# Kernel tuning notes

Hardware: AMD Instinct MI355X
Metric: run time of the kernel (lower is better)

## Reference

```python
import jax, jax.numpy as jnp
import numpy as np

N_NODES = 50000
N_EDGES = 800000
D = 128          # input_dim == output_dim
H = 2 * D        # hidden size = 2*output_dim
EPS = 1e-5       # BatchNorm1d eps


def _mlp(x, W1, b1, g1, beta1, W2, b2):
    # Linear -> BatchNorm1d (training-mode batch stats) -> ReLU -> Linear
    y = x @ W1 + b1
    mu = jnp.mean(y, axis=0)
    var = jnp.mean(jnp.square(y - mu), axis=0)  # biased var, as used for normalization
    y = (y - mu) * jax.lax.rsqrt(var + EPS) * g1 + beta1
    y = jax.nn.relu(y)
    return y @ W2 + b2


def setup_inputs() -> dict:
    key = jax.random.key(0)
    ks = jax.random.split(key, 16)
    h = jax.random.normal(ks[0], (N_NODES, D), dtype=jnp.float32)
    e = jax.random.normal(ks[1], (N_EDGES, D), dtype=jnp.float32)
    src = jax.random.randint(ks[2], (N_EDGES,), 0, N_NODES, dtype=jnp.int32)
    dst = jax.random.randint(ks[3], (N_EDGES,), 0, N_NODES, dtype=jnp.int32)

    def lin(k, fan_in, fan_out):
        return jax.random.normal(k, (fan_in, fan_out), dtype=jnp.float32) * (1.0 / np.sqrt(fan_in))

    params = {
        # mlp_bond: in 2D -> H -> D
        'W1b': lin(ks[4], 2 * D, H), 'b1b': jnp.zeros((H,), jnp.float32),
        'g1b': jnp.ones((H,), jnp.float32), 'beta1b': jnp.zeros((H,), jnp.float32),
        'W2b': lin(ks[5], H, D), 'b2b': jnp.zeros((D,), jnp.float32),
        # mlp_atom: in 2D -> H -> D
        'W1a': lin(ks[6], 2 * D, H), 'b1a': jnp.zeros((H,), jnp.float32),
        'g1a': jnp.ones((H,), jnp.float32), 'beta1a': jnp.zeros((H,), jnp.float32),
        'W2a': lin(ks[7], H, D), 'b2a': jnp.zeros((D,), jnp.float32),
    }
    return {'h': h, 'e': e, 'src': src, 'dst': dst, **params}


def reference(h, e, src, dst,
              W1b, b1b, g1b, beta1b, W2b, b2b,
              W1a, b1a, g1a, beta1a, W2a, b2a):
    # --- bond update: gather u_add_v, concat with e, MLP ---
    sum_h_edge = h[src] + h[dst]                              # [E, D]
    e_new = _mlp(jnp.concatenate([sum_h_edge, e], axis=-1),
                 W1b, b1b, g1b, beta1b, W2b, b2b)             # [E, D]

    # --- atom update: scatter-sum of src node feats and NEW edge feats to dst ---
    sum_h = jax.ops.segment_sum(h[src], dst, num_segments=N_NODES)   # copy_u + sum
    sum_e = jax.ops.segment_sum(e_new, dst, num_segments=N_NODES)   # copy_e + sum
    h_new = _mlp(jnp.concatenate([sum_h, sum_e], axis=-1),
                 W1a, b1a, g1a, beta1a, W2a, b2a)             # [N, D]

    # out_batch_norm=False, out_activation=None, residual=False, dropout=None
    return h_new, e_new
```

## Files before the change

kernel.cpp:

```cpp
#include <hip/hip_runtime.h>
#include <stdint.h>

#define DD 128
#define HH 256
#define EPSBN 1e-5f

typedef __attribute__((ext_vector_type(4))) float f32x4;
typedef __attribute__((ext_vector_type(8))) short s16x8;
typedef __attribute__((ext_vector_type(4))) short s16x4;

__device__ __forceinline__ unsigned short f2bf(float f){
  union{float f; unsigned u;} v; v.f=f;
  unsigned u = v.u + 0x7fffu + ((v.u>>16)&1u);
  return (unsigned short)(u>>16);
}
__device__ __forceinline__ float bf2f(unsigned short s){
  union{unsigned u; float f;} v; v.u=((unsigned)s)<<16; return v.f;
}
__device__ __forceinline__ int swz(int row, int kb){ return row*512 + (kb ^ ((row&7)<<4)); }

__global__ void wt_kernel(const float* __restrict__ W1b, const float* __restrict__ W2b,
                          const float* __restrict__ W1a, const float* __restrict__ W2a,
                          unsigned short* __restrict__ WT1b, unsigned short* __restrict__ WT2b,
                          unsigned short* __restrict__ WT1a, unsigned short* __restrict__ WT2a){
  int idx = blockIdx.x*256 + threadIdx.x;
  if (idx < 65536){ int n=idx>>8, k=idx&255; WT1b[n*256+k]=f2bf(W1b[k*256+n]); }
  else if (idx < 98304){ int t=idx-65536; int n=t>>8, k=t&255; WT2b[n*256+k]=f2bf(W2b[k*128+n]); }
  else if (idx < 163840){ int t=idx-98304; int n=t>>8, k=t&255; WT1a[n*256+k]=f2bf(W1a[k*256+n]); }
  else if (idx < 196608){ int t=idx-163840; int n=t>>8, k=t&255; WT2a[n*256+k]=f2bf(W2a[k*128+n]); }
}

__global__ void h2bf_kernel(const float* __restrict__ h, unsigned short* __restrict__ hb, int n8){
  int i = blockIdx.x*256 + threadIdx.x;
  if (i < n8){
    f32x4 a = *(const f32x4*)(h + (size_t)i*8);
    f32x4 b = *(const f32x4*)(h + (size_t)i*8 + 4);
    s16x8 p;
    #pragma unroll
    for (int q=0;q<4;q++){ p[q]=(short)f2bf(a[q]); p[4+q]=(short)f2bf(b[q]); }
    *(s16x8*)(hb + (size_t)i*8) = p;
  }
}

__global__ void hist_kernel(const int* __restrict__ dst, int* __restrict__ counts, int E){
  int i = blockIdx.x*256 + threadIdx.x;
  if (i < E) atomicAdd(&counts[dst[i]], 1);
}

__global__ void scan_kernel(const int* __restrict__ counts, int* __restrict__ offsets,
                            int* __restrict__ cursor, int n){
  __shared__ int wsum[16];
  int tid = threadIdx.x, lane = tid&63, wid = tid>>6;
  int carry = 0;
  int nch = (n + 1023)/1024;
  for (int ch=0; ch<nch; ch++){
    int i = ch*1024 + tid;
    int v = (i<n)? counts[i] : 0;
    int s = v;
    #pragma unroll
    for (int off=1; off<64; off<<=1){ int t = __shfl_up(s, off); if (lane>=off) s += t; }
    if (lane==63) wsum[wid] = s;
    __syncthreads();
    int woff = 0, tot = 0;
    #pragma unroll
    for (int w=0; w<16; w++){ int t = wsum[w]; if (w<wid) woff += t; tot += t; }
    if (i<n){ int excl = carry + woff + s - v; offsets[i]=excl; cursor[i]=excl; }
    carry += tot;
    __syncthreads();
  }
  if (tid==0) offsets[n] = carry;
}

__global__ void fill_kernel(const int* __restrict__ dst, int* __restrict__ cursor,
                            int* __restrict__ eids, int E){
  int i = blockIdx.x*256 + threadIdx.x;
  if (i < E){ int slot = atomicAdd(&cursor[dst[i]], 1); eids[slot] = i; }
}

__device__ __forceinline__ void gemm1_core(char* xt, const s16x8 (&Bf)[8][2],
                                           float bias0, float bias1,
                                           unsigned short* __restrict__ yout,
                                           float* __restrict__ stats,
                                           int base, int nrows)
{
  const int tid = threadIdx.x;
  const int l = tid&63, w = tid>>6, lr = l&15, lg = l>>4;
  const int nb = w*32;
  f32x4 acc[4][2];
  #pragma unroll
  for (int mt=0;mt<4;mt++)
    #pragma unroll
    for (int nt=0;nt<2;nt++) acc[mt][nt] = (f32x4){0.f,0.f,0.f,0.f};
  #pragma unroll
  for (int kc=0;kc<8;kc++){
    s16x8 af[4];
    #pragma unroll
    for (int mt=0;mt<4;mt++)
      af[mt] = *(const s16x8*)(xt + swz(mt*16 + lr, kc*64 + lg*16));
    #pragma unroll
    for (int nt=0;nt<2;nt++)
      #pragma unroll
      for (int mt=0;mt<4;mt++)
        acc[mt][nt] = __builtin_amdgcn_mfma_f32_16x16x32_bf16(af[mt], Bf[kc][nt], acc[mt][nt], 0,0,0);
  }
  float st1a=0.f, st1b=0.f, st2a=0.f, st2b=0.f;
  #pragma unroll
  for (int mt=0;mt<4;mt++)
    #pragma unroll
    for (int q=0;q<4;q++){
      float m = (base + mt*16 + lg*4 + q < nrows) ? 1.0f : 0.0f;
      float v0 = (acc[mt][0][q] + bias0)*m;
      float v1 = (acc[mt][1][q] + bias1)*m;
      st1a += v0; st2a += v0*v0;
      st1b += v1; st2b += v1*v1;
    }
  __syncthreads();
  #pragma unroll
  for (int mt=0;mt<4;mt++)
    #pragma unroll
    for (int q=0;q<4;q++){
      *(unsigned short*)(xt + (mt*16 + lg*4 + q)*512 + (nb + lr)*2)      = f2bf(acc[mt][0][q] + bias0);
      *(unsigned short*)(xt + (mt*16 + lg*4 + q)*512 + (nb + 16 + lr)*2) = f2bf(acc[mt][1][q] + bias1);
    }
  __syncthreads();
  #pragma unroll
  for (int it=0;it<4;it++){
    int off = it*8192 + tid*16;
    int row = off >> 9;
    if (base + row < nrows)
      *(s16x8*)((char*)yout + (size_t)base*512 + off) = *(const s16x8*)(xt + off);
  }
  {
    int rep = blockIdx.x & 63;
    float s;
    s = st1a; s += __shfl_xor(s,16); s += __shfl_xor(s,32);
    if (l < 16) atomicAdd(&stats[rep*512 + nb + lr], s);
    s = st2a; s += __shfl_xor(s,16); s += __shfl_xor(s,32);
    if (l < 16) atomicAdd(&stats[rep*512 + 256 + nb + lr], s);
    s = st1b; s += __shfl_xor(s,16); s += __shfl_xor(s,32);
    if (l < 16) atomicAdd(&stats[rep*512 + nb + 16 + lr], s);
    s = st2b; s += __shfl_xor(s,16); s += __shfl_xor(s,32);
    if (l < 16) atomicAdd(&stats[rep*512 + 256 + nb + 16 + lr], s);
  }
}

__global__ __launch_bounds__(512, 4) void edge_mlp1(
    const unsigned short* __restrict__ hb, const float* __restrict__ e,
    const int* __restrict__ src, const int* __restrict__ dstv,
    const unsigned short* __restrict__ WT1, const float* __restrict__ b1,
    unsigned short* __restrict__ yout, float* __restrict__ stats, int E)
{
  __shared__ alignas(16) char xt[32768];
  const int tid = threadIdx.x;
  const int l = tid&63, w = tid>>6, lr = l&15, lg = l>>4;
  const int nb = w*32;
  const int base = blockIdx.x*64;

  {
    const int cb = tid&31, r0 = tid>>5;
    #pragma unroll
    for (int k=0;k<4;k++){
      int r = r0 + k*16;
      f32x4 v = *(const f32x4*)(e + (size_t)(base+r)*DD + cb*4);
      s16x4 p;
      #pragma unroll
      for (int q=0;q<4;q++) p[q] = (short)f2bf(v[q]);
      *(s16x4*)(xt + swz(r, 256 + cb*8)) = p;
    }
  }
  {
    const int r = tid>>3, jj = tid&7;
    const int ei = base + r;
    int s_ = src[ei], d_ = dstv[ei];
    const s16x8* hs = (const s16x8*)(hb + (size_t)s_*DD) + jj*2;
    const s16x8* hd = (const s16x8*)(hb + (size_t)d_*DD) + jj*2;
    s16x8 a0=hs[0], a1=hs[1], c0=hd[0], c1=hd[1];
    s16x8 o0, o1;
    #pragma unroll
    for (int q=0;q<8;q++){
      o0[q] = (short)f2bf(bf2f((unsigned short)a0[q]) + bf2f((unsigned short)c0[q]));
      o1[q] = (short)f2bf(bf2f((unsigned short)a1[q]) + bf2f((unsigned short)c1[q]));
    }
    *(s16x8*)(xt + swz(r, jj*32))      = o0;
    *(s16x8*)(xt + swz(r, jj*32 + 16)) = o1;
  }
  s16x8 Bf[8][2];
  #pragma unroll
  for (int kc=0;kc<8;kc++)
    #pragma unroll
    for (int nt=0;nt<2;nt++)
      Bf[kc][nt] = *(const s16x8*)(WT1 + (size_t)(nb + nt*16 + lr)*256 + kc*32 + lg*8);
  float bias0 = b1[nb+lr], bias1 = b1[nb+16+lr];
  __syncthreads();
  gemm1_core(xt, Bf, bias0, bias1, yout, stats, base, E);
}

__global__ __launch_bounds__(512, 2) void node_mlp1(
    const unsigned short* __restrict__ hb, const float* __restrict__ enew,
    const int* __restrict__ src, const int* __restrict__ offsets, const int* __restrict__ eids,
    const unsigned short* __restrict__ WT1, const float* __restrict__ b1,
    unsigned short* __restrict__ yout, float* __restrict__ stats, int NN)
{
  __shared__ alignas(16) char xt[32768];
  const int tid = threadIdx.x;
  const int l = tid&63, w = tid>>6, lr = l&15, lg = l>>4;
  const int nb = w*32;
  const int base = blockIdx.x*64;
  const int r = tid>>3, jj = tid&7;
  const int node = base + r;

  float ah[16], ae[16];
  #pragma unroll
  for (int q=0;q<16;q++){ ah[q]=0.f; ae[q]=0.f; }
  if (node < NN){
    int beg = offsets[node], end = offsets[node+1];
    for (int p=beg;p<end;p++){
      int eid = eids[p];
      int s_ = src[eid];
      const s16x8* hs = (const s16x8*)(hb + (size_t)s_*DD + jj*16);
      const f32x4* ep = (const f32x4*)(enew + (size_t)eid*DD + jj*16);
      s16x8 a0 = hs[0], a1 = hs[1];
      f32x4 e0 = ep[0], e1 = ep[1], e2 = ep[2], e3 = ep[3];
      #pragma unroll
      for (int q=0;q<8;q++){ ah[q] += bf2f((unsigned short)a0[q]); ah[8+q] += bf2f((unsigned short)a1[q]); }
      #pragma unroll
      for (int q=0;q<4;q++){ ae[q] += e0[q]; ae[4+q] += e1[q]; ae[8+q] += e2[q]; ae[12+q] += e3[q]; }
    }
  }
  {
    s16x8 o0, o1;
    #pragma unroll
    for (int q=0;q<8;q++){ o0[q] = (short)f2bf(ah[q]); o1[q] = (short)f2bf(ah[8+q]); }
    *(s16x8*)(xt + swz(r, jj*32))      = o0;
    *(s16x8*)(xt + swz(r, jj*32 + 16)) = o1;
    #pragma unroll
    for (int q=0;q<8;q++){ o0[q] = (short)f2bf(ae[q]); o1[q] = (short)f2bf(ae[8+q]); }
    *(s16x8*)(xt + swz(r, 256 + jj*32))      = o0;
    *(s16x8*)(xt + swz(r, 256 + jj*32 + 16)) = o1;
  }
  s16x8 Bf[8][2];
  #pragma unroll
  for (int kc=0;kc<8;kc++)
    #pragma unroll
    for (int nt=0;nt<2;nt++)
      Bf[kc][nt] = *(const s16x8*)(WT1 + (size_t)(nb + nt*16 + lr)*256 + kc*32 + lg*8);
  float bias0 = b1[nb+lr], bias1 = b1[nb+16+lr];
  __syncthreads();
  gemm1_core(xt, Bf, bias0, bias1, yout, stats, base, NN);
}

__global__ void finalize_kernel(const float* __restrict__ stats, const float* __restrict__ g,
                                const float* __restrict__ beta, float* __restrict__ scale, float invcnt){
  __shared__ float red[512];
  int tid = threadIdx.x;
  float s = 0.f;
  for (int rep=0; rep<64; rep++) s += stats[rep*512 + tid];
  red[tid] = s;
  __syncthreads();
  if (tid < 256){
    float mu  = red[tid]*invcnt;
    float var = red[256+tid]*invcnt - mu*mu;
    float a = g[tid] * rsqrtf(var + EPSBN);
    float c = beta[tid] - mu*a;
    scale[2*tid] = a; scale[2*tid+1] = c;
  }
}

__global__ __launch_bounds__(512, 4) void mlp2_kernel(const unsigned short* y,
    const unsigned short* __restrict__ WT2, const float* __restrict__ b2,
    const float* __restrict__ scale, float* outp, int nrows)
{
  __shared__ alignas(16) char xt[32768];
  const int tid = threadIdx.x;
  const int l = tid&63, w = tid>>6, lr = l&15, lg = l>>4;
  const int nb = w*16;
  const int base = blockIdx.x*64;

  const int cb = tid&31, r0 = tid>>5;
  float sa[8], sc[8];
  #pragma unroll
  for (int q=0;q<8;q++){ sa[q]=scale[2*(cb*8+q)]; sc[q]=scale[2*(cb*8+q)+1]; }
  #pragma unroll
  for (int k=0;k<4;k++){
    int r = r0 + k*16;
    s16x8 raw = {0,0,0,0,0,0,0,0};
    if (base + r < nrows) raw = *(const s16x8*)(y + (size_t)(base+r)*HH + cb*8);
    s16x8 o;
    #pragma unroll
    for (int q=0;q<8;q++){
      float f = fmaxf(bf2f((unsigned short)raw[q])*sa[q] + sc[q], 0.0f);
      o[q] = (short)f2bf(f);
    }
    *(s16x8*)(xt + swz(r, cb*16)) = o;
  }
  s16x8 Bf[8];
  #pragma unroll
  for (int kc=0;kc<8;kc++)
    Bf[kc] = *(const s16x8*)(WT2 + (size_t)(nb + lr)*HH + kc*32 + lg*8);
  float bias = b2[nb+lr];
  __syncthreads();

  f32x4 acc[4];
  #pragma unroll
  for (int mt=0;mt<4;mt++) acc[mt] = (f32x4){0.f,0.f,0.f,0.f};
  #pragma unroll
  for (int kc=0;kc<8;kc++){
    s16x8 af[4];
    #pragma unroll
    for (int mt=0;mt<4;mt++)
      af[mt] = *(const s16x8*)(xt + swz(mt*16 + lr, kc*64 + lg*16));
    #pragma unroll
    for (int mt=0;mt<4;mt++)
      acc[mt] = __builtin_amdgcn_mfma_f32_16x16x32_bf16(af[mt], Bf[kc], acc[mt], 0,0,0);
  }
  __syncthreads();
  #pragma unroll
  for (int mt=0;mt<4;mt++)
    #pragma unroll
    for (int q=0;q<4;q++)
      *(float*)(xt + (mt*16 + lg*4 + q)*512 + (nb + lr)*4) = acc[mt][q] + bias;
  __syncthreads();
  #pragma unroll
  for (int it=0;it<4;it++){
    int off = it*8192 + tid*16;
    int row = off >> 9;
    if (base + row < nrows)
      *(f32x4*)(outp + (size_t)(base+row)*DD + ((off&511)>>2)) = *(const f32x4*)(xt + off);
  }
}

extern "C" void kernel_launch(void* const* d_in, const int* in_sizes, int n_in,
                              void* d_out, int out_size, void* d_ws, size_t ws_size,
                              hipStream_t stream) {
  const float* h    = (const float*)d_in[0];
  const float* e    = (const float*)d_in[1];
  const int*   src  = (const int*)d_in[2];
  const int*   dst  = (const int*)d_in[3];
  const float* W1b  = (const float*)d_in[4];
  const float* b1b  = (const float*)d_in[5];
  const float* g1b  = (const float*)d_in[6];
  const float* beta1b=(const float*)d_in[7];
  const float* W2b  = (const float*)d_in[8];
  const float* b2b  = (const float*)d_in[9];
  const float* W1a  = (const float*)d_in[10];
  const float* b1a  = (const float*)d_in[11];
  const float* g1a  = (const float*)d_in[12];
  const float* beta1a=(const float*)d_in[13];
  const float* W2a  = (const float*)d_in[14];
  const float* b2a  = (const float*)d_in[15];

  const int E  = in_sizes[2];
  const int NN = in_sizes[0] / DD;

  char* ws = (char*)d_ws;
  unsigned short* WT1b = (unsigned short*)(ws + 0);
  unsigned short* WT2b = (unsigned short*)(ws + 131072);
  unsigned short* WT1a = (unsigned short*)(ws + 196608);
  unsigned short* WT2a = (unsigned short*)(ws + 327680);
  float* scaleE = (float*)(ws + 393216);
  float* scaleN = (float*)(ws + 395264);
  float* statsE = (float*)(ws + 397312);
  float* statsN = (float*)(ws + 528384);
  int* counts  = (int*)(ws + 659456);
  int* offsets = (int*)(ws + 860160);
  int* cursor  = (int*)(ws + 1060864);
  int* eids    = (int*)(ws + 1261568);
  unsigned short* ya = (unsigned short*)(ws + 4461568);
  unsigned short* hb = (unsigned short*)(ws + 30086144);

  float* outH = (float*)d_out;
  float* outE = outH + (size_t)NN * DD;
  unsigned short* yE = (unsigned short*)outE;

  hipMemsetAsync(ws + 397312, 0, 131072 + 131072 + 200704, stream);

  wt_kernel<<<768, 256, 0, stream>>>(W1b, W2b, W1a, W2a, WT1b, WT2b, WT1a, WT2a);
  h2bf_kernel<<<(NN*DD/8 + 255)/256, 256, 0, stream>>>(h, hb, NN*DD/8);
  hist_kernel<<<(E+255)/256, 256, 0, stream>>>(dst, counts, E);
  scan_kernel<<<1, 1024, 0, stream>>>(counts, offsets, cursor, NN);
  fill_kernel<<<(E+255)/256, 256, 0, stream>>>(dst, cursor, eids, E);

  const int tE = E/64;
  const int tN = (NN + 63)/64;

  edge_mlp1<<<tE, 512, 0, stream>>>(hb, e, src, dst, WT1b, b1b, yE, statsE, E);
  finalize_kernel<<<1, 512, 0, stream>>>(statsE, g1b, beta1b, scaleE, 1.0f/(float)E);
  mlp2_kernel<<<tE, 512, 0, stream>>>(yE, WT2b, b2b, scaleE, outE, E);
  node_mlp1<<<tN, 512, 0, stream>>>(hb, outE, src, offsets, eids, WT1a, b1a, ya, statsN, NN);
  finalize_kernel<<<1, 512, 0, stream>>>(statsN, g1a, beta1a, scaleN, 1.0f/(float)NN);
  mlp2_kernel<<<tN, 512, 0, stream>>>(ya, WT2a, b2a, scaleN, outH, NN);
}
```

Baseline: 800.5 us.

## Recompute edge GEMM1 instead of storing hidden; fuse MLP2 with atomic scatter-sum

The edge MLP now runs in two passes. The first pass computes only the BatchNorm statistics of the first linear layer. The second pass recomputes the gather and GEMM1, then applies BN, ReLU and GEMM2 in one fused kernel. It writes e_new and atomically scatter-adds it into a per-node sum buffer, so the node kernel no longer gathers e_new per edge. This drops the bf16 hidden-activation round trip and the CSR gather of edge features, at the cost of a duplicated gather plus GEMM1 and 800k×128 float atomics. It also swaps the manual bf16 rounding for the library conversion.

```diff
diff --git a/kernel.cpp b/kernel.cpp
--- a/kernel.cpp
+++ b/kernel.cpp
@@ -1,4 +1,5 @@
 #include <hip/hip_runtime.h>
+#include <hip/hip_bf16.h>
 #include <stdint.h>
 
 #define DD 128
@@ -10,9 +11,9 @@
 typedef __attribute__((ext_vector_type(4))) short s16x4;
 
 __device__ __forceinline__ unsigned short f2bf(float f){
-  union{float f; unsigned u;} v; v.f=f;
-  unsigned u = v.u + 0x7fffu + ((v.u>>16)&1u);
-  return (unsigned short)(u>>16);
+  union { __hip_bfloat16 h; unsigned short u; } v;
+  v.h = __float2bfloat16(f);
+  return v.u;
 }
 __device__ __forceinline__ float bf2f(unsigned short s){
   union{unsigned u; float f;} v; v.u=((unsigned)s)<<16; return v.f;
@@ -75,6 +76,199 @@
                             int* __restrict__ eids, int E){
   int i = blockIdx.x*256 + threadIdx.x;
   if (i < E){ int slot = atomicAdd(&cursor[dst[i]], 1); eids[slot] = i; }
+}
+
+__device__ __forceinline__ void stage_edge_tile(char* xt,
+    const unsigned short* __restrict__ hb, const float* __restrict__ e,
+    const int* __restrict__ src, const int* __restrict__ dstv, int base)
+{
+  const int tid = threadIdx.x;
+  {
+    const int cb = tid&31, r0 = tid>>5;
+    #pragma unroll
+    for (int k=0;k<4;k++){
+      int r = r0 + k*16;
+      f32x4 v = *(const f32x4*)(e + (size_t)(base+r)*DD + cb*4);
+      s16x4 p;
+      #pragma unroll
+      for (int q=0;q<4;q++) p[q] = (short)f2bf(v[q]);
+      *(s16x4*)(xt + swz(r, 256 + cb*8)) = p;
+    }
+  }
+  {
+    const int r = tid>>3, jj = tid&7;
+    const int ei = base + r;
+    int s_ = src[ei], d_ = dstv[ei];
+    const s16x8* hs = (const s16x8*)(hb + (size_t)s_*DD) + jj*2;
+    const s16x8* hd = (const s16x8*)(hb + (size_t)d_*DD) + jj*2;
+    s16x8 a0=hs[0], a1=hs[1], c0=hd[0], c1=hd[1];
+    s16x8 o0, o1;
+    #pragma unroll
+    for (int q=0;q<8;q++){
+      o0[q] = (short)f2bf(bf2f((unsigned short)a0[q]) + bf2f((unsigned short)c0[q]));
+      o1[q] = (short)f2bf(bf2f((unsigned short)a1[q]) + bf2f((unsigned short)c1[q]));
+    }
+    *(s16x8*)(xt + swz(r, jj*32))      = o0;
+    *(s16x8*)(xt + swz(r, jj*32 + 16)) = o1;
+  }
+}
+
+__global__ __launch_bounds__(512, 4) void edge_stats(
+    const unsigned short* __restrict__ hb, const float* __restrict__ e,
+    const int* __restrict__ src, const int* __restrict__ dstv,
+    const unsigned short* __restrict__ WT1, const float* __restrict__ b1,
+    float* __restrict__ stats, int E)
+{
+  __shared__ alignas(16) char xt[32768];
+  const int tid = threadIdx.x;
+  const int l = tid&63, w = tid>>6, lr = l&15, lg = l>>4;
+  const int nb = w*32;
+  const int base = blockIdx.x*64;
+
+  stage_edge_tile(xt, hb, e, src, dstv, base);
+
+  s16x8 Bf[8][2];
+  #pragma unroll
+  for (int kc=0;kc<8;kc++)
+    #pragma unroll
+    for (int nt=0;nt<2;nt++)
+      Bf[kc][nt] = *(const s16x8*)(WT1 + (size_t)(nb + nt*16 + lr)*256 + kc*32 + lg*8);
+  float bias0 = b1[nb+lr], bias1 = b1[nb+16+lr];
+  __syncthreads();
+
+  f32x4 acc[4][2];
+  #pragma unroll
+  for (int mt=0;mt<4;mt++)
+    #pragma unroll
+    for (int nt=0;nt<2;nt++) acc[mt][nt] = (f32x4){0.f,0.f,0.f,0.f};
+  #pragma unroll
+  for (int kc=0;kc<8;kc++){
+    s16x8 af[4];
+    #pragma unroll
+    for (int mt=0;mt<4;mt++)
+      af[mt] = *(const s16x8*)(xt + swz(mt*16 + lr, kc*64 + lg*16));
+    #pragma unroll
+    for (int nt=0;nt<2;nt++)
+      #pragma unroll
+      for (int mt=0;mt<4;mt++)
+        acc[mt][nt] = __builtin_amdgcn_mfma_f32_16x16x32_bf16(af[mt], Bf[kc][nt], acc[mt][nt], 0,0,0);
+  }
+  float st1a=0.f, st1b=0.f, st2a=0.f, st2b=0.f;
+  #pragma unroll
+  for (int mt=0;mt<4;mt++)
+    #pragma unroll
+    for (int q=0;q<4;q++){
+      float v0 = acc[mt][0][q] + bias0;
+      float v1 = acc[mt][1][q] + bias1;
+      st1a += v0; st2a += v0*v0;
+      st1b += v1; st2b += v1*v1;
+    }
+  int rep = blockIdx.x & 63;
+  float s;
+  s = st1a; s += __shfl_xor(s,16); s += __shfl_xor(s,32);
+  if (l < 16) atomicAdd(&stats[rep*512 + nb + lr], s);
+  s = st2a; s += __shfl_xor(s,16); s += __shfl_xor(s,32);
+  if (l < 16) atomicAdd(&stats[rep*512 + 256 + nb + lr], s);
+  s = st1b; s += __shfl_xor(s,16); s += __shfl_xor(s,32);
+  if (l < 16) atomicAdd(&stats[rep*512 + nb + 16 + lr], s);
+  s = st2b; s += __shfl_xor(s,16); s += __shfl_xor(s,32);
+  if (l < 16) atomicAdd(&stats[rep*512 + 256 + nb + 16 + lr], s);
+}
+
+__global__ __launch_bounds__(512, 2) void edge_fused(
+    const unsigned short* __restrict__ hb, const float* __restrict__ e,
+    const int* __restrict__ src, const int* __restrict__ dstv,
+    const unsigned short* __restrict__ WT1, const float* __restrict__ b1,
+    const unsigned short* __restrict__ WT2, const float* __restrict__ b2,
+    const float* __restrict__ scale, float* __restrict__ outp,
+    float* __restrict__ sumE, int E)
+{
+  __shared__ alignas(16) char xt[32768];
+  const int tid = threadIdx.x;
+  const int l = tid&63, w = tid>>6, lr = l&15, lg = l>>4;
+  const int nb = w*32;
+  const int nb2 = w*16;
+  const int base = blockIdx.x*64;
+
+  stage_edge_tile(xt, hb, e, src, dstv, base);
+
+  s16x8 Bf[8][2];
+  #pragma unroll
+  for (int kc=0;kc<8;kc++)
+    #pragma unroll
+    for (int nt=0;nt<2;nt++)
+      Bf[kc][nt] = *(const s16x8*)(WT1 + (size_t)(nb + nt*16 + lr)*256 + kc*32 + lg*8);
+  float bias0 = b1[nb+lr], bias1 = b1[nb+16+lr];
+  float a0 = scale[2*(nb+lr)],    c0 = scale[2*(nb+lr)+1];
+  float a1 = scale[2*(nb+16+lr)], c1 = scale[2*(nb+16+lr)+1];
+  s16x8 Bf2[8];
+  #pragma unroll
+  for (int kc=0;kc<8;kc++)
+    Bf2[kc] = *(const s16x8*)(WT2 + (size_t)(nb2 + lr)*HH + kc*32 + lg*8);
+  float bias2 = b2[nb2+lr];
+  __syncthreads();
+
+  f32x4 acc[4][2];
+  #pragma unroll
+  for (int mt=0;mt<4;mt++)
+    #pragma unroll
+    for (int nt=0;nt<2;nt++) acc[mt][nt] = (f32x4){0.f,0.f,0.f,0.f};
+  #pragma unroll
+  for (int kc=0;kc<8;kc++){
+    s16x8 af[4];
+    #pragma unroll
+    for (int mt=0;mt<4;mt++)
+      af[mt] = *(const s16x8*)(xt + swz(mt*16 + lr, kc*64 + lg*16));
+    #pragma unroll
+    for (int nt=0;nt<2;nt++)
+      #pragma unroll
+      for (int mt=0;mt<4;mt++)
+        acc[mt][nt] = __builtin_amdgcn_mfma_f32_16x16x32_bf16(af[mt], Bf[kc][nt], acc[mt][nt], 0,0,0);
+  }
+  __syncthreads();
+  #pragma unroll
+  for (int mt=0;mt<4;mt++)
+    #pragma unroll
+    for (int q=0;q<4;q++){
+      int row = mt*16 + lg*4 + q;
+      float v0 = fmaxf((acc[mt][0][q] + bias0)*a0 + c0, 0.f);
+      float v1 = fmaxf((acc[mt][1][q] + bias1)*a1 + c1, 0.f);
+      *(unsigned short*)(xt + swz(row, (nb + lr)*2))      = f2bf(v0);
+      *(unsigned short*)(xt + swz(row, (nb + 16 + lr)*2)) = f2bf(v1);
+    }
+  __syncthreads();
+  f32x4 acc2[4];
+  #pragma unroll
+  for (int mt=0;mt<4;mt++) acc2[mt] = (f32x4){0.f,0.f,0.f,0.f};
+  #pragma unroll
+  for (int kc=0;kc<8;kc++){
+    s16x8 af[4];
+    #pragma unroll
+    for (int mt=0;mt<4;mt++)
+      af[mt] = *(const s16x8*)(xt + swz(mt*16 + lr, kc*64 + lg*16));
+    #pragma unroll
+    for (int mt=0;mt<4;mt++)
+      acc2[mt] = __builtin_amdgcn_mfma_f32_16x16x32_bf16(af[mt], Bf2[kc], acc2[mt], 0,0,0);
+  }
+  __syncthreads();
+  #pragma unroll
+  for (int mt=0;mt<4;mt++)
+    #pragma unroll
+    for (int q=0;q<4;q++)
+      *(float*)(xt + (mt*16 + lg*4 + q)*512 + (nb2 + lr)*4) = acc2[mt][q] + bias2;
+  __syncthreads();
+  #pragma unroll
+  for (int it=0;it<4;it++){
+    int off = it*8192 + tid*16;
+    int row = off >> 9;
+    int col = (off & 511) >> 2;
+    f32x4 v = *(const f32x4*)(xt + off);
+    *(f32x4*)(outp + (size_t)(base+row)*DD + col) = v;
+    int d = dstv[base+row];
+    float* sp = sumE + (size_t)d*DD + col;
+    atomicAdd(sp+0, v[0]); atomicAdd(sp+1, v[1]);
+    atomicAdd(sp+2, v[2]); atomicAdd(sp+3, v[3]);
+  }
 }
 
 __device__ __forceinline__ void gemm1_core(char* xt, const s16x8 (&Bf)[8][2],
@@ -144,59 +338,8 @@
   }
 }
 
-__global__ __launch_bounds__(512, 4) void edge_mlp1(
-    const unsigned short* __restrict__ hb, const float* __restrict__ e,
-    const int* __restrict__ src, const int* __restrict__ dstv,
-    const unsigned short* __restrict__ WT1, const float* __restrict__ b1,
-    unsigned short* __restrict__ yout, float* __restrict__ stats, int E)
-{
-  __shared__ alignas(16) char xt[32768];
-  const int tid = threadIdx.x;
-  const int l = tid&63, w = tid>>6, lr = l&15, lg = l>>4;
-  const int nb = w*32;
-  const int base = blockIdx.x*64;
-
-  {
-    const int cb = tid&31, r0 = tid>>5;
-    #pragma unroll
-    for (int k=0;k<4;k++){
-      int r = r0 + k*16;
-      f32x4 v = *(const f32x4*)(e + (size_t)(base+r)*DD + cb*4);
-      s16x4 p;
-      #pragma unroll
-      for (int q=0;q<4;q++) p[q] = (short)f2bf(v[q]);
-      *(s16x4*)(xt + swz(r, 256 + cb*8)) = p;
-    }
-  }
-  {
-    const int r = tid>>3, jj = tid&7;
-    const int ei = base + r;
-    int s_ = src[ei], d_ = dstv[ei];
-    const s16x8* hs = (const s16x8*)(hb + (size_t)s_*DD) + jj*2;
-    const s16x8* hd = (const s16x8*)(hb + (size_t)d_*DD) + jj*2;
-    s16x8 a0=hs[0], a1=hs[1], c0=hd[0], c1=hd[1];
-    s16x8 o0, o1;
-    #pragma unroll
-    for (int q=0;q<8;q++){
-      o0[q] = (short)f2bf(bf2f((unsigned short)a0[q]) + bf2f((unsigned short)c0[q]));
-      o1[q] = (short)f2bf(bf2f((unsigned short)a1[q]) + bf2f((unsigned short)c1[q]));
-    }
-    *(s16x8*)(xt + swz(r, jj*32))      = o0;
-    *(s16x8*)(xt + swz(r, jj*32 + 16)) = o1;
-  }
-  s16x8 Bf[8][2];
-  #pragma unroll
-  for (int kc=0;kc<8;kc++)
-    #pragma unroll
-    for (int nt=0;nt<2;nt++)
-      Bf[kc][nt] = *(const s16x8*)(WT1 + (size_t)(nb + nt*16 + lr)*256 + kc*32 + lg*8);
-  float bias0 = b1[nb+lr], bias1 = b1[nb+16+lr];
-  __syncthreads();
-  gemm1_core(xt, Bf, bias0, bias1, yout, stats, base, E);
-}
-
 __global__ __launch_bounds__(512, 2) void node_mlp1(
-    const unsigned short* __restrict__ hb, const float* __restrict__ enew,
+    const unsigned short* __restrict__ hb, const float* __restrict__ sumE,
     const int* __restrict__ src, const int* __restrict__ offsets, const int* __restrict__ eids,
     const unsigned short* __restrict__ WT1, const float* __restrict__ b1,
     unsigned short* __restrict__ yout, float* __restrict__ stats, int NN)
@@ -209,23 +352,22 @@
   const int r = tid>>3, jj = tid&7;
   const int node = base + r;
 
-  float ah[16], ae[16];
-  #pragma unroll
-  for (int q=0;q<16;q++){ ah[q]=0.f; ae[q]=0.f; }
+  float ah[16];
+  #pragma unroll
+  for (int q=0;q<16;q++) ah[q]=0.f;
+  f32x4 ae0={0,0,0,0}, ae1={0,0,0,0}, ae2={0,0,0,0}, ae3={0,0,0,0};
   if (node < NN){
     int beg = offsets[node], end = offsets[node+1];
     for (int p=beg;p<end;p++){
       int eid = eids[p];
       int s_ = src[eid];
       const s16x8* hs = (const s16x8*)(hb + (size_t)s_*DD + jj*16);
-      const f32x4* ep = (const f32x4*)(enew + (size_t)eid*DD + jj*16);
       s16x8 a0 = hs[0], a1 = hs[1];
-      f32x4 e0 = ep[0], e1 = ep[1], e2 = ep[2], e3 = ep[3];
       #pragma unroll
       for (int q=0;q<8;q++){ ah[q] += bf2f((unsigned short)a0[q]); ah[8+q] += bf2f((unsigned short)a1[q]); }
-      #pragma unroll
-      for (int q=0;q<4;q++){ ae[q] += e0[q]; ae[4+q] += e1[q]; ae[8+q] += e2[q]; ae[12+q] += e3[q]; }
-    }
+    }
+    const f32x4* ep = (const f32x4*)(sumE + (size_t)node*DD + jj*16);
+    ae0 = ep[0]; ae1 = ep[1]; ae2 = ep[2]; ae3 = ep[3];
   }
   {
     s16x8 o0, o1;
@@ -234,7 +376,10 @@
     *(s16x8*)(xt + swz(r, jj*32))      = o0;
     *(s16x8*)(xt + swz(r, jj*32 + 16)) = o1;
     #pragma unroll
-    for (int q=0;q<8;q++){ o0[q] = (short)f2bf(ae[q]); o1[q] = (short)f2bf(ae[8+q]); }
+    for (int q=0;q<4;q++){
+      o0[q]   = (short)f2bf(ae0[q]); o0[4+q] = (short)f2bf(ae1[q]);
+      o1[q]   = (short)f2bf(ae2[q]); o1[4+q] = (short)f2bf(ae3[q]);
+    }
     *(s16x8*)(xt + swz(r, 256 + jj*32))      = o0;
     *(s16x8*)(xt + swz(r, 256 + jj*32 + 16)) = o1;
   }
@@ -370,9 +515,10 @@
 
   float* outH = (float*)d_out;
   float* outE = outH + (size_t)NN * DD;
-  unsigned short* yE = (unsigned short*)outE;
+  float* sumE = outH;
 
   hipMemsetAsync(ws + 397312, 0, 131072 + 131072 + 200704, stream);
+  hipMemsetAsync((void*)sumE, 0, (size_t)NN * DD * sizeof(float), stream);
 
   wt_kernel<<<768, 256, 0, stream>>>(W1b, W2b, W1a, W2a, WT1b, WT2b, WT1a, WT2a);
   h2bf_kernel<<<(NN*DD/8 + 255)/256, 256, 0, stream>>>(h, hb, NN*DD/8);
@@ -383,10 +529,11 @@
   const int tE = E/64;
   const int tN = (NN + 63)/64;
 
-  edge_mlp1<<<tE, 512, 0, stream>>>(hb, e, src, dst, WT1b, b1b, yE, statsE, E);
+  edge_stats<<<tE, 512, 0, stream>>>(hb, e, src, dst, WT1b, b1b, statsE, E);
   finalize_kernel<<<1, 512, 0, stream>>>(statsE, g1b, beta1b, scaleE, 1.0f/(float)E);
-  mlp2_kernel<<<tE, 512, 0, stream>>>(yE, WT2b, b2b, scaleE, outE, E);
-  node_mlp1<<<tN, 512, 0, stream>>>(hb, outE, src, offsets, eids, WT1a, b1a, ya, statsN, NN);
+  edge_fused<<<tE, 512, 0, stream>>>(hb, e, src, dst, WT1b, b1b, WT2b, b2b,
+                                     scaleE, outE, sumE, E);
+  node_mlp1<<<tN, 512, 0, stream>>>(hb, sumE, src, offsets, eids, WT1a, b1a, ya, statsN, NN);
   finalize_kernel<<<1, 512, 0, stream>>>(statsN, g1a, beta1a, scaleN, 1.0f/(float)NN);
   mlp2_kernel<<<tN, 512, 0, stream>>>(ya, WT2a, b2a, scaleN, outH, NN);
 }
```

Measured after the change: 1.926 ms. +140.6%, slower.

## Shrink edge MLP and mlp2 tiles to 32 rows with 256-thread blocks

Applied to the files above, without the earlier changes.

The edge first-layer GEMM and both second-layer GEMM kernels now use 32-row tiles and 256-thread blocks. The edge kernel loops over two halves of the hidden dimension, reloading weight fragments for each half, and stages the bf16 output in shared memory before writing it out. The aim is more blocks in flight and better latency hiding for the gather-heavy edge path. The cost is twice as many blocks doing BN-stat atomics and more weight-fragment reloads per row. The LDS swizzle is widened to 32 rows, and bf16 conversion now uses the HIP intrinsic.

```diff
diff --git a/kernel.cpp b/kernel.cpp
--- a/kernel.cpp
+++ b/kernel.cpp
@@ -1,4 +1,5 @@
 #include <hip/hip_runtime.h>
+#include <hip/hip_bf16.h>
 #include <stdint.h>
 
 #define DD 128
@@ -10,14 +11,14 @@
 typedef __attribute__((ext_vector_type(4))) short s16x4;
 
 __device__ __forceinline__ unsigned short f2bf(float f){
-  union{float f; unsigned u;} v; v.f=f;
-  unsigned u = v.u + 0x7fffu + ((v.u>>16)&1u);
-  return (unsigned short)(u>>16);
+  union { __hip_bfloat16 h; unsigned short u; } v;
+  v.h = __float2bfloat16(f);
+  return v.u;
 }
 __device__ __forceinline__ float bf2f(unsigned short s){
   union{unsigned u; float f;} v; v.u=((unsigned)s)<<16; return v.f;
 }
-__device__ __forceinline__ int swz(int row, int kb){ return row*512 + (kb ^ ((row&7)<<4)); }
+__device__ __forceinline__ int swz(int row, int kb){ return row*512 + (kb ^ ((row&31)<<4)); }
 
 __global__ void wt_kernel(const float* __restrict__ W1b, const float* __restrict__ W2b,
                           const float* __restrict__ W1a, const float* __restrict__ W2a,
@@ -75,6 +76,181 @@
                             int* __restrict__ eids, int E){
   int i = blockIdx.x*256 + threadIdx.x;
   if (i < E){ int slot = atomicAdd(&cursor[dst[i]], 1); eids[slot] = i; }
+}
+
+__global__ __launch_bounds__(256, 4) void edge_mlp1(
+    const unsigned short* __restrict__ hb, const float* __restrict__ e,
+    const int* __restrict__ src, const int* __restrict__ dstv,
+    const unsigned short* __restrict__ WT1, const float* __restrict__ b1,
+    unsigned short* __restrict__ yout, float* __restrict__ stats, int E)
+{
+  __shared__ alignas(16) char xt[32768];
+  char* yl = xt + 16384;
+  const int tid = threadIdx.x;
+  const int l = tid&63, w = tid>>6, lr = l&15, lg = l>>4;
+  const int base = blockIdx.x*32;
+
+  {
+    const int cb = tid&31, r0 = tid>>5;
+    #pragma unroll
+    for (int k=0;k<4;k++){
+      int r = r0 + k*8;
+      f32x4 v = *(const f32x4*)(e + (size_t)(base+r)*DD + cb*4);
+      s16x4 p;
+      #pragma unroll
+      for (int q=0;q<4;q++) p[q] = (short)f2bf(v[q]);
+      *(s16x4*)(xt + swz(r, 256 + cb*8)) = p;
+    }
+  }
+  {
+    const int r = tid>>3, jj = tid&7;
+    const int ei = base + r;
+    int s_ = src[ei], d_ = dstv[ei];
+    const s16x8* hs = (const s16x8*)(hb + (size_t)s_*DD) + jj*2;
+    const s16x8* hd = (const s16x8*)(hb + (size_t)d_*DD) + jj*2;
+    s16x8 a0=hs[0], a1=hs[1], c0=hd[0], c1=hd[1];
+    s16x8 o0, o1;
+    #pragma unroll
+    for (int q=0;q<8;q++){
+      o0[q] = (short)f2bf(bf2f((unsigned short)a0[q]) + bf2f((unsigned short)c0[q]));
+      o1[q] = (short)f2bf(bf2f((unsigned short)a1[q]) + bf2f((unsigned short)c1[q]));
+    }
+    *(s16x8*)(xt + swz(r, jj*32))      = o0;
+    *(s16x8*)(xt + swz(r, jj*32 + 16)) = o1;
+  }
+  __syncthreads();
+
+  const int rep = blockIdx.x & 63;
+  #pragma unroll 1
+  for (int half=0; half<2; half++){
+    const int nbh = half*128 + w*32;
+    s16x8 Bf[8][2];
+    #pragma unroll
+    for (int kc=0;kc<8;kc++)
+      #pragma unroll
+      for (int nt=0;nt<2;nt++)
+        Bf[kc][nt] = *(const s16x8*)(WT1 + (size_t)(nbh + nt*16 + lr)*256 + kc*32 + lg*8);
+    float bias0 = b1[nbh+lr], bias1 = b1[nbh+16+lr];
+
+    f32x4 acc[2][2];
+    #pragma unroll
+    for (int mt=0;mt<2;mt++)
+      #pragma unroll
+      for (int nt=0;nt<2;nt++) acc[mt][nt] = (f32x4){0.f,0.f,0.f,0.f};
+    #pragma unroll
+    for (int kc=0;kc<8;kc++){
+      s16x8 af[2];
+      #pragma unroll
+      for (int mt=0;mt<2;mt++)
+        af[mt] = *(const s16x8*)(xt + swz(mt*16 + lr, kc*64 + lg*16));
+      #pragma unroll
+      for (int nt=0;nt<2;nt++)
+        #pragma unroll
+        for (int mt=0;mt<2;mt++)
+          acc[mt][nt] = __builtin_amdgcn_mfma_f32_16x16x32_bf16(af[mt], Bf[kc][nt], acc[mt][nt], 0,0,0);
+    }
+    float st1a=0.f, st1b=0.f, st2a=0.f, st2b=0.f;
+    #pragma unroll
+    for (int mt=0;mt<2;mt++)
+      #pragma unroll
+      for (int q=0;q<4;q++){
+        float v0 = acc[mt][0][q] + bias0;
+        float v1 = acc[mt][1][q] + bias1;
+        st1a += v0; st2a += v0*v0;
+        st1b += v1; st2b += v1*v1;
+        int row = mt*16 + lg*4 + q;
+        *(unsigned short*)(yl + row*512 + (nbh + lr)*2)      = f2bf(v0);
+        *(unsigned short*)(yl + row*512 + (nbh + 16 + lr)*2) = f2bf(v1);
+      }
+    float s;
+    s = st1a; s += __shfl_xor(s,16); s += __shfl_xor(s,32);
+    if (l < 16) atomicAdd(&stats[rep*512 + nbh + lr], s);
+    s = st2a; s += __shfl_xor(s,16); s += __shfl_xor(s,32);
+    if (l < 16) atomicAdd(&stats[rep*512 + 256 + nbh + lr], s);
+    s = st1b; s += __shfl_xor(s,16); s += __shfl_xor(s,32);
+    if (l < 16) atomicAdd(&stats[rep*512 + nbh + 16 + lr], s);
+    s = st2b; s += __shfl_xor(s,16); s += __shfl_xor(s,32);
+    if (l < 16) atomicAdd(&stats[rep*512 + 256 + nbh + 16 + lr], s);
+  }
+  __syncthreads();
+  #pragma unroll
+  for (int it=0;it<4;it++){
+    int off = it*4096 + tid*16;
+    *(s16x8*)((char*)yout + (size_t)base*512 + off) = *(const s16x8*)(yl + off);
+  }
+}
+
+__global__ __launch_bounds__(256, 4) void mlp2_kernel(const unsigned short* y,
+    const unsigned short* __restrict__ WT2, const float* __restrict__ b2,
+    const float* __restrict__ scale, float* outp, int nrows)
+{
+  __shared__ alignas(16) char xt[16384];
+  const int tid = threadIdx.x;
+  const int l = tid&63, w = tid>>6, lr = l&15, lg = l>>4;
+  const int nb = w*32;
+  const int base = blockIdx.x*32;
+
+  {
+    const int cb = tid&31, r0 = tid>>5;
+    float sa[8], sc[8];
+    #pragma unroll
+    for (int q=0;q<8;q++){ sa[q]=scale[2*(cb*8+q)]; sc[q]=scale[2*(cb*8+q)+1]; }
+    #pragma unroll
+    for (int k=0;k<4;k++){
+      int r = r0 + k*8;
+      s16x8 raw = {0,0,0,0,0,0,0,0};
+      if (base + r < nrows) raw = *(const s16x8*)(y + (size_t)(base+r)*HH + cb*8);
+      s16x8 o;
+      #pragma unroll
+      for (int q=0;q<8;q++){
+        float f = fmaxf(bf2f((unsigned short)raw[q])*sa[q] + sc[q], 0.0f);
+        o[q] = (short)f2bf(f);
+      }
+      *(s16x8*)(xt + swz(r, cb*16)) = o;
+    }
+  }
+  s16x8 Bf[8][2];
+  #pragma unroll
+  for (int kc=0;kc<8;kc++)
+    #pragma unroll
+    for (int nt=0;nt<2;nt++)
+      Bf[kc][nt] = *(const s16x8*)(WT2 + (size_t)(nb + nt*16 + lr)*HH + kc*32 + lg*8);
+  float bias0 = b2[nb+lr], bias1 = b2[nb+16+lr];
+  __syncthreads();
+
+  f32x4 acc[2][2];
+  #pragma unroll
+  for (int mt=0;mt<2;mt++)
+    #pragma unroll
+    for (int nt=0;nt<2;nt++) acc[mt][nt] = (f32x4){0.f,0.f,0.f,0.f};
+  #pragma unroll
+  for (int kc=0;kc<8;kc++){
+    s16x8 af[2];
+    #pragma unroll
+    for (int mt=0;mt<2;mt++)
+      af[mt] = *(const s16x8*)(xt + swz(mt*16 + lr, kc*64 + lg*16));
+    #pragma unroll
+    for (int nt=0;nt<2;nt++)
+      #pragma unroll
+      for (int mt=0;mt<2;mt++)
+        acc[mt][nt] = __builtin_amdgcn_mfma_f32_16x16x32_bf16(af[mt], Bf[kc][nt], acc[mt][nt], 0,0,0);
+  }
+  __syncthreads();
+  #pragma unroll
+  for (int mt=0;mt<2;mt++)
+    #pragma unroll
+    for (int nt=0;nt<2;nt++)
+      #pragma unroll
+      for (int q=0;q<4;q++)
+        *(float*)(xt + (mt*16 + lg*4 + q)*512 + (nb + nt*16 + lr)*4) = acc[mt][nt][q] + (nt ? bias1 : bias0);
+  __syncthreads();
+  #pragma unroll
+  for (int it=0;it<4;it++){
+    int off = it*4096 + tid*16;
+    int row = off >> 9;
+    if (base + row < nrows)
+      *(f32x4*)(outp + (size_t)(base+row)*DD + ((off&511)>>2)) = *(const f32x4*)(xt + off);
+  }
 }
 
 __device__ __forceinline__ void gemm1_core(char* xt, const s16x8 (&Bf)[8][2],
@@ -142,57 +318,6 @@
     s = st2b; s += __shfl_xor(s,16); s += __shfl_xor(s,32);
     if (l < 16) atomicAdd(&stats[rep*512 + 256 + nb + 16 + lr], s);
   }
-}
-
-__global__ __launch_bounds__(512, 4) void edge_mlp1(
-    const unsigned short* __restrict__ hb, const float* __restrict__ e,
-    const int* __restrict__ src, const int* __restrict__ dstv,
-    const unsigned short* __restrict__ WT1, const float* __restrict__ b1,
-    unsigned short* __restrict__ yout, float* __restrict__ stats, int E)
-{
-  __shared__ alignas(16) char xt[32768];
-  const int tid = threadIdx.x;
-  const int l = tid&63, w = tid>>6, lr = l&15, lg = l>>4;
-  const int nb = w*32;
-  const int base = blockIdx.x*64;
-
-  {
-    const int cb = tid&31, r0 = tid>>5;
-    #pragma unroll
-    for (int k=0;k<4;k++){
-      int r = r0 + k*16;
-      f32x4 v = *(const f32x4*)(e + (size_t)(base+r)*DD + cb*4);
-      s16x4 p;
-      #pragma unroll
-      for (int q=0;q<4;q++) p[q] = (short)f2bf(v[q]);
-      *(s16x4*)(xt + swz(r, 256 + cb*8)) = p;
-    }
-  }
-  {
-    const int r = tid>>3, jj = tid&7;
-    const int ei = base + r;
-    int s_ = src[ei], d_ = dstv[ei];
-    const s16x8* hs = (const s16x8*)(hb + (size_t)s_*DD) + jj*2;
-    const s16x8* hd = (const s16x8*)(hb + (size_t)d_*DD) + jj*2;
-    s16x8 a0=hs[0], a1=hs[1], c0=hd[0], c1=hd[1];
-    s16x8 o0, o1;
-    #pragma unroll
-    for (int q=0;q<8;q++){
-      o0[q] = (short)f2bf(bf2f((unsigned short)a0[q]) + bf2f((unsigned short)c0[q]));
-      o1[q] = (short)f2bf(bf2f((unsigned short)a1[q]) + bf2f((unsigned short)c1[q]));
-    }
-    *(s16x8*)(xt + swz(r, jj*32))      = o0;
-    *(s16x8*)(xt + swz(r, jj*32 + 16)) = o1;
-  }
-  s16x8 Bf[8][2];
-  #pragma unroll
-  for (int kc=0;kc<8;kc++)
-    #pragma unroll
-    for (int nt=0;nt<2;nt++)
-      Bf[kc][nt] = *(const s16x8*)(WT1 + (size_t)(nb + nt*16 + lr)*256 + kc*32 + lg*8);
-  float bias0 = b1[nb+lr], bias1 = b1[nb+16+lr];
-  __syncthreads();
-  gemm1_core(xt, Bf, bias0, bias1, yout, stats, base, E);
 }
 
 __global__ __launch_bounds__(512, 2) void node_mlp1(
@@ -263,69 +388,6 @@
     float a = g[tid] * rsqrtf(var + EPSBN);
     float c = beta[tid] - mu*a;
     scale[2*tid] = a; scale[2*tid+1] = c;
-  }
-}
-
-__global__ __launch_bounds__(512, 4) void mlp2_kernel(const unsigned short* y,
-    const unsigned short* __restrict__ WT2, const float* __restrict__ b2,
-    const float* __restrict__ scale, float* outp, int nrows)
-{
-  __shared__ alignas(16) char xt[32768];
-  const int tid = threadIdx.x;
-  const int l = tid&63, w = tid>>6, lr = l&15, lg = l>>4;
-  const int nb = w*16;
-  const int base = blockIdx.x*64;
-
-  const int cb = tid&31, r0 = tid>>5;
-  float sa[8], sc[8];
-  #pragma unroll
-  for (int q=0;q<8;q++){ sa[q]=scale[2*(cb*8+q)]; sc[q]=scale[2*(cb*8+q)+1]; }
-  #pragma unroll
-  for (int k=0;k<4;k++){
-    int r = r0 + k*16;
-    s16x8 raw = {0,0,0,0,0,0,0,0};
-    if (base + r < nrows) raw = *(const s16x8*)(y + (size_t)(base+r)*HH + cb*8);
-    s16x8 o;
-    #pragma unroll
-    for (int q=0;q<8;q++){
-      float f = fmaxf(bf2f((unsigned short)raw[q])*sa[q] + sc[q], 0.0f);
-      o[q] = (short)f2bf(f);
-    }
-    *(s16x8*)(xt + swz(r, cb*16)) = o;
-  }
-  s16x8 Bf[8];
-  #pragma unroll
-  for (int kc=0;kc<8;kc++)
-    Bf[kc] = *(const s16x8*)(WT2 + (size_t)(nb + lr)*HH + kc*32 + lg*8);
-  float bias = b2[nb+lr];
-  __syncthreads();
-
-  f32x4 acc[4];
-  #pragma unroll
-  for (int mt=0;mt<4;mt++) acc[mt] = (f32x4){0.f,0.f,0.f,0.f};
-  #pragma unroll
-  for (int kc=0;kc<8;kc++){
-    s16x8 af[4];
-    #pragma unroll
-    for (int mt=0;mt<4;mt++)
-      af[mt] = *(const s16x8*)(xt + swz(mt*16 + lr, kc*64 + lg*16));
-    #pragma unroll
-    for (int mt=0;mt<4;mt++)
-      acc[mt] = __builtin_amdgcn_mfma_f32_16x16x32_bf16(af[mt], Bf[kc], acc[mt], 0,0,0);
-  }
-  __syncthreads();
-  #pragma unroll
-  for (int mt=0;mt<4;mt++)
-    #pragma unroll
-    for (int q=0;q<4;q++)
-      *(float*)(xt + (mt*16 + lg*4 + q)*512 + (nb + lr)*4) = acc[mt][q] + bias;
-  __syncthreads();
-  #pragma unroll
-  for (int it=0;it<4;it++){
-    int off = it*8192 + tid*16;
-    int row = off >> 9;
-    if (base + row < nrows)
-      *(f32x4*)(outp + (size_t)(base+row)*DD + ((off&511)>>2)) = *(const f32x4*)(xt + off);
   }
 }
 
@@ -380,13 +442,14 @@
   scan_kernel<<<1, 1024, 0, stream>>>(counts, offsets, cursor, NN);
   fill_kernel<<<(E+255)/256, 256, 0, stream>>>(dst, cursor, eids, E);
 
-  const int tE = E/64;
-  const int tN = (NN + 63)/64;
-
-  edge_mlp1<<<tE, 512, 0, stream>>>(hb, e, src, dst, WT1b, b1b, yE, statsE, E);
+  const int tE32 = E/32;
+  const int tN64 = (NN + 63)/64;
+  const int tN32 = (NN + 31)/32;
+
+  edge_mlp1<<<tE32, 256, 0, stream>>>(hb, e, src, dst, WT1b, b1b, yE, statsE, E);
   finalize_kernel<<<1, 512, 0, stream>>>(statsE, g1b, beta1b, scaleE, 1.0f/(float)E);
-  mlp2_kernel<<<tE, 512, 0, stream>>>(yE, WT2b, b2b, scaleE, outE, E);
-  node_mlp1<<<tN, 512, 0, stream>>>(hb, outE, src, offsets, eids, WT1a, b1a, ya, statsN, NN);
+  mlp2_kernel<<<tE32, 256, 0, stream>>>(yE, WT2b, b2b, scaleE, outE, E);
+  node_mlp1<<<tN64, 512, 0, stream>>>(hb, outE, src, offsets, eids, WT1a, b1a, ya, statsN, NN);
   finalize_kernel<<<1, 512, 0, stream>>>(statsN, g1a, beta1a, scaleN, 1.0f/(float)NN);
-  mlp2_kernel<<<tN, 512, 0, stream>>>(ya, WT2a, b2a, scaleN, outH, NN);
-}
+  mlp2_kernel<<<tN32, 256, 0, stream>>>(ya, WT2a, b2a, scaleN, outH, NN);
+}
```

New measurement: 1.053 ms. 1.32x slower.
